# Kernel tuning notes

Hardware: AMD Instinct MI355X
Metric: run time of the kernel (lower is better)

Reference implementation:

```python
import jax, jax.numpy as jnp
import numpy as np

N_PAIRS = 1_600_000   # total neighbor pairs (len(idx_i))
N_ATOMS = 50_000      # number of distinct center atoms (avg 32 neighbors each)


def setup_inputs() -> dict:
    key = jax.random.key(0)
    # sorted center indices -> consecutive ragged segments, like a neighbor list
    idx_i = jnp.sort(jax.random.randint(key, (N_PAIRS,), 0, N_ATOMS, dtype=jnp.int32))
    return {"idx_i": idx_i}


def reference(idx_i):
    # NOTE: output shape is data-dependent (sum_i C(c_i,2)), so this runs eagerly
    # (the concrete sizes below are python ints pulled from the input values),
    # exactly mirroring torch.unique_consecutive + per-segment torch.combinations.
    n = idx_i.shape[0]
    # --- unique_consecutive(return_counts=True), vectorized ---
    change = jnp.concatenate([jnp.ones((1,), bool), idx_i[1:] != idx_i[:-1]])
    seg_id = jnp.cumsum(change.astype(jnp.int32)) - 1          # [n] segment id per pair
    n_seg = int(seg_id[-1]) + 1
    counts = jnp.bincount(seg_id, length=n_seg)                 # [n_seg] c_i
    seg_off = jnp.concatenate([jnp.zeros((1,), counts.dtype), jnp.cumsum(counts)[:-1]])
    # --- per-segment number of unordered pairs C(c,2) ---
    tri_counts = counts * (counts - 1) // 2
    tri_off = jnp.concatenate([jnp.zeros((1,), tri_counts.dtype), jnp.cumsum(tri_counts)[:-1]])
    T = int(jnp.sum(tri_counts))
    # --- one flat vectorized pass over all T triples ---
    idx_i_triples = jnp.repeat(jnp.arange(n_seg, dtype=jnp.int32), tri_counts,
                               total_repeat_length=T)           # [T] segment index
    r = jnp.arange(T, dtype=counts.dtype) - tri_off[idx_i_triples]  # local triple rank
    c = counts[idx_i_triples]                                   # segment size per triple
    M = c * (c - 1) // 2
    rr = M - 1 - r                                              # rank counted from the end
    # triangular-root decode of condensed upper-triangle index (c is small -> fp32 exact)
    a_rev = jnp.floor((jnp.sqrt(8.0 * rr.astype(jnp.float32) + 1.0) - 1.0) / 2.0).astype(c.dtype)
    a = c - 2 - a_rev                                           # first local neighbor pos
    b = c - 1 - (rr - a_rev * (a_rev + 1) // 2)                 # second local neighbor pos (> a)
    base = seg_off[idx_i_triples]
    idx_j_triples = base + a
    idx_k_triples = base + b
    return (idx_i_triples, idx_j_triples, idx_k_triples)
```

## Files before the change

kernel.cpp:

```cpp
#include <hip/hip_runtime.h>

#define THREADS 256

__global__ void k_count_starts(const int* __restrict__ idx, int n, int E,
                               int* __restrict__ blockCounts) {
    int base = (blockIdx.x * THREADS + threadIdx.x) * E;
    int cnt = 0;
    for (int j = 0; j < E; ++j) {
        int p = base + j;
        if (p < n) {
            int v = idx[p];
            cnt += (p == 0) || (idx[p - 1] != v);
        }
    }
    __shared__ int sd[THREADS];
    sd[threadIdx.x] = cnt;
    __syncthreads();
    for (int off = THREADS >> 1; off > 0; off >>= 1) {
        if (threadIdx.x < off) sd[threadIdx.x] += sd[threadIdx.x + off];
        __syncthreads();
    }
    if (threadIdx.x == 0) blockCounts[blockIdx.x] = sd[0];
}

__global__ void k_scan1024(const int* __restrict__ in, int nb,
                           int* __restrict__ outExcl,
                           int* __restrict__ totalOut,
                           int* __restrict__ tailArr, int tailVal) {
    __shared__ int sc[1024];
    int tid = threadIdx.x;
    int v = (tid < nb) ? in[tid] : 0;
    sc[tid] = v;
    __syncthreads();
    for (int off = 1; off < 1024; off <<= 1) {
        int t = 0;
        if (tid >= off) t = sc[tid - off];
        __syncthreads();
        if (tid >= off) sc[tid] += t;
        __syncthreads();
    }
    if (tid < nb) outExcl[tid] = sc[tid] - v;
    if (tid == 1023) {
        int total = sc[1023];
        if (totalOut) *totalOut = total;
        if (tailArr) tailArr[total] = tailVal;
    }
}

__global__ void k_emit_starts(const int* __restrict__ idx, int n, int E,
                              const int* __restrict__ blockOffs,
                              int* __restrict__ segOff) {
    int tid = threadIdx.x;
    int base = (blockIdx.x * THREADS + tid) * E;
    int cnt = 0;
    for (int j = 0; j < E; ++j) {
        int p = base + j;
        if (p < n) cnt += (p == 0) || (idx[p - 1] != idx[p]);
    }
    __shared__ int sc[THREADS];
    sc[tid] = cnt;
    __syncthreads();
    for (int off = 1; off < THREADS; off <<= 1) {
        int t = 0;
        if (tid >= off) t = sc[tid - off];
        __syncthreads();
        if (tid >= off) sc[tid] += t;
        __syncthreads();
    }
    int myOff = blockOffs[blockIdx.x] + sc[tid] - cnt;
    for (int j = 0; j < E; ++j) {
        int p = base + j;
        if (p < n && ((p == 0) || (idx[p - 1] != idx[p]))) segOff[myOff++] = p;
    }
}

__global__ void k_tri_blocksums(const int* __restrict__ segOff,
                                const int* __restrict__ nsegPtr, int E,
                                int* __restrict__ triBlockSums) {
    int nseg = *nsegPtr;
    int base = (blockIdx.x * THREADS + threadIdx.x) * E;
    int sum = 0;
    for (int j = 0; j < E; ++j) {
        int s = base + j;
        if (s < nseg) {
            int c = segOff[s + 1] - segOff[s];
            sum += c * (c - 1) / 2;
        }
    }
    __shared__ int sd[THREADS];
    sd[threadIdx.x] = sum;
    __syncthreads();
    for (int off = THREADS >> 1; off > 0; off >>= 1) {
        if (threadIdx.x < off) sd[threadIdx.x] += sd[threadIdx.x + off];
        __syncthreads();
    }
    if (threadIdx.x == 0) triBlockSums[blockIdx.x] = sd[0];
}

__global__ void k_emit_trioff(const int* __restrict__ segOff,
                              const int* __restrict__ nsegPtr, int E,
                              const int* __restrict__ triBlockOffs,
                              int* __restrict__ triOff) {
    int nseg = *nsegPtr;
    int tid = threadIdx.x;
    int base = (blockIdx.x * THREADS + tid) * E;
    int cnt = 0;
    for (int j = 0; j < E; ++j) {
        int s = base + j;
        if (s < nseg) {
            int c = segOff[s + 1] - segOff[s];
            cnt += c * (c - 1) / 2;
        }
    }
    __shared__ int sc[THREADS];
    sc[tid] = cnt;
    __syncthreads();
    for (int off = 1; off < THREADS; off <<= 1) {
        int t = 0;
        if (tid >= off) t = sc[tid - off];
        __syncthreads();
        if (tid >= off) sc[tid] += t;
        __syncthreads();
    }
    int run = triBlockOffs[blockIdx.x] + sc[tid] - cnt;
    for (int j = 0; j < E; ++j) {
        int s = base + j;
        if (s < nseg) {
            int c = segOff[s + 1] - segOff[s];
            triOff[s] = run;
            run += c * (c - 1) / 2;
        }
    }
}

__global__ void k_fill(const int* __restrict__ segOff,
                       const int* __restrict__ triOff,
                       const int* __restrict__ nsegPtr,
                       int* __restrict__ outI, int* __restrict__ outJ,
                       int* __restrict__ outK) {
    int nseg = *nsegPtr;
    for (int s = blockIdx.x; s < nseg; s += gridDim.x) {
        int baseP = segOff[s];
        int c = segOff[s + 1] - baseP;
        int M = c * (c - 1) / 2;
        int t0 = triOff[s];
        for (int r = threadIdx.x; r < M; r += THREADS) {
            int rr = M - 1 - r;
            int k = (int)floorf((sqrtf((float)(8 * rr + 1)) - 1.0f) * 0.5f);
            if (k < 0) k = 0;
            while ((k + 1) * (k + 2) / 2 <= rr) ++k;
            while (k * (k + 1) / 2 > rr) --k;
            int a = c - 2 - k;
            int b = c - 1 - (rr - k * (k + 1) / 2);
            int t = t0 + r;
            outI[t] = s;
            outJ[t] = baseP + a;
            outK[t] = baseP + b;
        }
    }
}

extern "C" void kernel_launch(void* const* d_in, const int* in_sizes, int n_in,
                              void* d_out, int out_size, void* d_ws, size_t ws_size,
                              hipStream_t stream) {
    const int* idx = (const int*)d_in[0];
    int n = in_sizes[0];
    int T = out_size / 3;
    int* out = (int*)d_out;
    int* ws = (int*)d_ws;

    int* nsegPtr      = ws;
    int* blockCounts  = ws + 16;
    int* blockOffs    = ws + 16 + 1024;
    int* triBlockSums = ws + 16 + 2048;
    int* triBlockOffs = ws + 16 + 3072;
    int* segOff       = ws + 16 + 4096;
    int* triOff       = segOff + (n + 1);

    int E = 8;
    while ((long long)(n + THREADS * E - 1) / (THREADS * E) > 1024) E <<= 1;
    int chunk = THREADS * E;
    int NB = (n + chunk - 1) / chunk;

    hipLaunchKernelGGL(k_count_starts, dim3(NB), dim3(THREADS), 0, stream,
                       idx, n, E, blockCounts);
    hipLaunchKernelGGL(k_scan1024, dim3(1), dim3(1024), 0, stream,
                       blockCounts, NB, blockOffs, nsegPtr, segOff, n);
    hipLaunchKernelGGL(k_emit_starts, dim3(NB), dim3(THREADS), 0, stream,
                       idx, n, E, blockOffs, segOff);
    hipLaunchKernelGGL(k_tri_blocksums, dim3(NB), dim3(THREADS), 0, stream,
                       segOff, nsegPtr, E, triBlockSums);
    hipLaunchKernelGGL(k_scan1024, dim3(1), dim3(1024), 0, stream,
                       triBlockSums, NB, triBlockOffs, (int*)nullptr,
                       (int*)nullptr, 0);
    hipLaunchKernelGGL(k_emit_trioff, dim3(NB), dim3(THREADS), 0, stream,
                       segOff, nsegPtr, E, triBlockOffs, triOff);
    hipLaunchKernelGGL(k_fill, dim3(4096), dim3(THREADS), 0, stream,
                       segOff, triOff, nsegPtr, out, out + T, out + 2 * T);
}
```

Measured before the change: 92.84 us.

## Drop separate scan kernels and assign one wavefront per segment in fill

Removes the two single-block 1024-thread scan launches. Each emit block now reduces the preceding chunk counts itself to get its prefix, and the last block writes the segment count and the tail sentinel. The fill kernel maps one 64-lane wavefront per segment instead of one 256-thread block, so fewer threads sit idle on segments with about 32 neighbors (about 500 triples each). The cost is that every emit block redundantly rereads up to NB chunk sums.

After: 86.04 us. 7.3% less time.

```diff
diff --git a/kernel.cpp b/kernel.cpp
--- a/kernel.cpp
+++ b/kernel.cpp
@@ -2,133 +2,127 @@
 
 #define THREADS 256
 
-__global__ void k_count_starts(const int* __restrict__ idx, int n, int E,
-                               int* __restrict__ blockCounts) {
-    int base = (blockIdx.x * THREADS + threadIdx.x) * E;
-    int cnt = 0;
-    for (int j = 0; j < E; ++j) {
-        int p = base + j;
-        if (p < n) {
-            int v = idx[p];
-            cnt += (p == 0) || (idx[p - 1] != v);
-        }
-    }
-    __shared__ int sd[THREADS];
-    sd[threadIdx.x] = cnt;
+__device__ __forceinline__ int blockReduceSum(int v, int* sdata) {
+    int tid = threadIdx.x;
+    sdata[tid] = v;
     __syncthreads();
     for (int off = THREADS >> 1; off > 0; off >>= 1) {
-        if (threadIdx.x < off) sd[threadIdx.x] += sd[threadIdx.x + off];
+        if (tid < off) sdata[tid] += sdata[tid + off];
         __syncthreads();
     }
-    if (threadIdx.x == 0) blockCounts[blockIdx.x] = sd[0];
+    int r = sdata[0];
+    __syncthreads();
+    return r;
 }
 
-__global__ void k_scan1024(const int* __restrict__ in, int nb,
-                           int* __restrict__ outExcl,
-                           int* __restrict__ totalOut,
-                           int* __restrict__ tailArr, int tailVal) {
-    __shared__ int sc[1024];
+__device__ __forceinline__ int blockScanIncl(int v, int* sdata) {
     int tid = threadIdx.x;
-    int v = (tid < nb) ? in[tid] : 0;
-    sc[tid] = v;
+    sdata[tid] = v;
     __syncthreads();
-    for (int off = 1; off < 1024; off <<= 1) {
+    for (int off = 1; off < THREADS; off <<= 1) {
         int t = 0;
-        if (tid >= off) t = sc[tid - off];
+        if (tid >= off) t = sdata[tid - off];
         __syncthreads();
-        if (tid >= off) sc[tid] += t;
+        if (tid >= off) sdata[tid] += t;
         __syncthreads();
     }
-    if (tid < nb) outExcl[tid] = sc[tid] - v;
-    if (tid == 1023) {
-        int total = sc[1023];
-        if (totalOut) *totalOut = total;
-        if (tailArr) tailArr[total] = tailVal;
-    }
+    int r = sdata[tid];
+    __syncthreads();
+    return r;
 }
 
-__global__ void k_emit_starts(const int* __restrict__ idx, int n, int E,
-                              const int* __restrict__ blockOffs,
-                              int* __restrict__ segOff) {
-    int tid = threadIdx.x;
-    int base = (blockIdx.x * THREADS + tid) * E;
+__global__ void k_count(const int* __restrict__ idx, int n, int E,
+                        int* __restrict__ chunkCnt) {
+    __shared__ int sdata[THREADS];
+    int base = (blockIdx.x * THREADS + threadIdx.x) * E;
     int cnt = 0;
     for (int j = 0; j < E; ++j) {
         int p = base + j;
         if (p < n) cnt += (p == 0) || (idx[p - 1] != idx[p]);
     }
-    __shared__ int sc[THREADS];
-    sc[tid] = cnt;
-    __syncthreads();
-    for (int off = 1; off < THREADS; off <<= 1) {
-        int t = 0;
-        if (tid >= off) t = sc[tid - off];
-        __syncthreads();
-        if (tid >= off) sc[tid] += t;
-        __syncthreads();
-    }
-    int myOff = blockOffs[blockIdx.x] + sc[tid] - cnt;
+    int tot = blockReduceSum(cnt, sdata);
+    if (threadIdx.x == 0) chunkCnt[blockIdx.x] = tot;
+}
+
+__global__ void k_emit_starts(const int* __restrict__ idx, int n, int E, int NB,
+                              const int* __restrict__ chunkCnt,
+                              int* __restrict__ segOff,
+                              int* __restrict__ nsegPtr) {
+    __shared__ int sdata[THREADS];
+    int tid = threadIdx.x;
+    int c = blockIdx.x;
+
+    int pv = 0;
+    for (int i = tid; i < c; i += THREADS) pv += chunkCnt[i];
+    int prefix = blockReduceSum(pv, sdata);
+
+    int base = (c * THREADS + tid) * E;
+    int cnt = 0;
     for (int j = 0; j < E; ++j) {
         int p = base + j;
-        if (p < n && ((p == 0) || (idx[p - 1] != idx[p]))) segOff[myOff++] = p;
+        if (p < n) cnt += (p == 0) || (idx[p - 1] != idx[p]);
+    }
+    int incl = blockScanIncl(cnt, sdata);
+    int off = prefix + incl - cnt;
+    for (int j = 0; j < E; ++j) {
+        int p = base + j;
+        if (p < n && ((p == 0) || (idx[p - 1] != idx[p]))) segOff[off++] = p;
+    }
+    if (c == NB - 1 && tid == THREADS - 1) {
+        int nseg = prefix + incl;
+        *nsegPtr = nseg;
+        segOff[nseg] = n;
     }
 }
 
-__global__ void k_tri_blocksums(const int* __restrict__ segOff,
-                                const int* __restrict__ nsegPtr, int E,
-                                int* __restrict__ triBlockSums) {
+__global__ void k_tri_sums(const int* __restrict__ segOff,
+                           const int* __restrict__ nsegPtr, int E,
+                           int* __restrict__ triChunkSum) {
+    __shared__ int sdata[THREADS];
     int nseg = *nsegPtr;
     int base = (blockIdx.x * THREADS + threadIdx.x) * E;
     int sum = 0;
     for (int j = 0; j < E; ++j) {
         int s = base + j;
         if (s < nseg) {
-            int c = segOff[s + 1] - segOff[s];
-            sum += c * (c - 1) / 2;
+            int cc = segOff[s + 1] - segOff[s];
+            sum += cc * (cc - 1) / 2;
         }
     }
-    __shared__ int sd[THREADS];
-    sd[threadIdx.x] = sum;
-    __syncthreads();
-    for (int off = THREADS >> 1; off > 0; off >>= 1) {
-        if (threadIdx.x < off) sd[threadIdx.x] += sd[threadIdx.x + off];
-        __syncthreads();
-    }
-    if (threadIdx.x == 0) triBlockSums[blockIdx.x] = sd[0];
+    int tot = blockReduceSum(sum, sdata);
+    if (threadIdx.x == 0) triChunkSum[blockIdx.x] = tot;
 }
 
 __global__ void k_emit_trioff(const int* __restrict__ segOff,
                               const int* __restrict__ nsegPtr, int E,
-                              const int* __restrict__ triBlockOffs,
+                              const int* __restrict__ triChunkSum,
                               int* __restrict__ triOff) {
+    __shared__ int sdata[THREADS];
     int nseg = *nsegPtr;
     int tid = threadIdx.x;
-    int base = (blockIdx.x * THREADS + tid) * E;
+    int c = blockIdx.x;
+
+    int pv = 0;
+    for (int i = tid; i < c; i += THREADS) pv += triChunkSum[i];
+    int prefix = blockReduceSum(pv, sdata);
+
+    int base = (c * THREADS + tid) * E;
     int cnt = 0;
     for (int j = 0; j < E; ++j) {
         int s = base + j;
         if (s < nseg) {
-            int c = segOff[s + 1] - segOff[s];
-            cnt += c * (c - 1) / 2;
+            int cc = segOff[s + 1] - segOff[s];
+            cnt += cc * (cc - 1) / 2;
         }
     }
-    __shared__ int sc[THREADS];
-    sc[tid] = cnt;
-    __syncthreads();
-    for (int off = 1; off < THREADS; off <<= 1) {
-        int t = 0;
-        if (tid >= off) t = sc[tid - off];
-        __syncthreads();
-        if (tid >= off) sc[tid] += t;
-        __syncthreads();
-    }
-    int run = triBlockOffs[blockIdx.x] + sc[tid] - cnt;
+    int incl = blockScanIncl(cnt, sdata);
+    int run = prefix + incl - cnt;
     for (int j = 0; j < E; ++j) {
         int s = base + j;
         if (s < nseg) {
-            int c = segOff[s + 1] - segOff[s];
+            int cc = segOff[s + 1] - segOff[s];
             triOff[s] = run;
-            run += c * (c - 1) / 2;
+            run += cc * (cc - 1) / 2;
         }
     }
 }
@@ -139,19 +133,22 @@
                        int* __restrict__ outI, int* __restrict__ outJ,
                        int* __restrict__ outK) {
     int nseg = *nsegPtr;
-    for (int s = blockIdx.x; s < nseg; s += gridDim.x) {
+    int wid = blockIdx.x * (THREADS / 64) + (threadIdx.x >> 6);
+    int lane = threadIdx.x & 63;
+    int nW = gridDim.x * (THREADS / 64);
+    for (int s = wid; s < nseg; s += nW) {
         int baseP = segOff[s];
-        int c = segOff[s + 1] - baseP;
-        int M = c * (c - 1) / 2;
+        int cc = segOff[s + 1] - baseP;
+        int M = cc * (cc - 1) / 2;
         int t0 = triOff[s];
-        for (int r = threadIdx.x; r < M; r += THREADS) {
+        for (int r = lane; r < M; r += 64) {
             int rr = M - 1 - r;
             int k = (int)floorf((sqrtf((float)(8 * rr + 1)) - 1.0f) * 0.5f);
             if (k < 0) k = 0;
             while ((k + 1) * (k + 2) / 2 <= rr) ++k;
             while (k * (k + 1) / 2 > rr) --k;
-            int a = c - 2 - k;
-            int b = c - 1 - (rr - k * (k + 1) / 2);
+            int a = cc - 2 - k;
+            int b = cc - 1 - (rr - k * (k + 1) / 2);
             int t = t0 + r;
             outI[t] = s;
             outJ[t] = baseP + a;
@@ -169,32 +166,25 @@
     int* out = (int*)d_out;
     int* ws = (int*)d_ws;
 
-    int* nsegPtr      = ws;
-    int* blockCounts  = ws + 16;
-    int* blockOffs    = ws + 16 + 1024;
-    int* triBlockSums = ws + 16 + 2048;
-    int* triBlockOffs = ws + 16 + 3072;
-    int* segOff       = ws + 16 + 4096;
-    int* triOff       = segOff + (n + 1);
+    int* nsegPtr     = ws;
+    int* chunkCnt    = ws + 16;
+    int* triChunkSum = ws + 16 + 1024;
+    int* segOff      = ws + 16 + 2048;
+    int* triOff      = segOff + (n + 1);
 
     int E = 8;
     while ((long long)(n + THREADS * E - 1) / (THREADS * E) > 1024) E <<= 1;
     int chunk = THREADS * E;
     int NB = (n + chunk - 1) / chunk;
 
-    hipLaunchKernelGGL(k_count_starts, dim3(NB), dim3(THREADS), 0, stream,
-                       idx, n, E, blockCounts);
-    hipLaunchKernelGGL(k_scan1024, dim3(1), dim3(1024), 0, stream,
-                       blockCounts, NB, blockOffs, nsegPtr, segOff, n);
+    hipLaunchKernelGGL(k_count, dim3(NB), dim3(THREADS), 0, stream,
+                       idx, n, E, chunkCnt);
     hipLaunchKernelGGL(k_emit_starts, dim3(NB), dim3(THREADS), 0, stream,
-                       idx, n, E, blockOffs, segOff);
-    hipLaunchKernelGGL(k_tri_blocksums, dim3(NB), dim3(THREADS), 0, stream,
-                       segOff, nsegPtr, E, triBlockSums);
-    hipLaunchKernelGGL(k_scan1024, dim3(1), dim3(1024), 0, stream,
-                       triBlockSums, NB, triBlockOffs, (int*)nullptr,
-                       (int*)nullptr, 0);
+                       idx, n, E, NB, chunkCnt, segOff, nsegPtr);
+    hipLaunchKernelGGL(k_tri_sums, dim3(NB), dim3(THREADS), 0, stream,
+                       segOff, nsegPtr, E, triChunkSum);
     hipLaunchKernelGGL(k_emit_trioff, dim3(NB), dim3(THREADS), 0, stream,
-                       segOff, nsegPtr, E, triBlockOffs, triOff);
+                       segOff, nsegPtr, E, triChunkSum, triOff);
     hipLaunchKernelGGL(k_fill, dim3(4096), dim3(THREADS), 0, stream,
                        segOff, triOff, nsegPtr, out, out + T, out + 2 * T);
 }
```
